# Kernel optimization log

Hardware: AMD Instinct MI355X
Metric: run time of the kernel (lower is better)

Reference implementation:

```python
import jax, jax.numpy as jnp
import numpy as np

N = 64
EPS = 1e-8


def setup_inputs() -> dict:
    key = jax.random.key(0)
    k1, k2, k3 = jax.random.split(key, 3)
    x = jax.random.normal(k1, (524288, N), dtype=jnp.float32)
    L = jax.random.uniform(k2, (2 * N, 2 * N), dtype=jnp.float32)
    R = jax.random.uniform(k3, (N, N), dtype=jnp.float32)
    return {"x": x, "L": L, "R": R}


def reference(x, L, R):
    n = N
    xr = x.reshape(n, -1)                      # (n, T)
    M = L @ L.T + EPS * jnp.eye(2 * n, dtype=L.dtype)
    M11 = M[:n, :n]
    M21 = M[:n, n:]   # note: original code names M[:n, n:] as M21
    M22 = M[n:, n:]
    A = 2.0 * (M11 + M22 + R - R.T)            # (n, n)
    A = jnp.linalg.inv(A) @ M21                # Koopman operator (n, n)
    return (A @ xr).reshape(-1, n)
```

## Files before the change

kernel.cpp:

```cpp
#include <hip/hip_runtime.h>

#define SN 524288

typedef float f32x4 __attribute__((ext_vector_type(4)));

__global__ __launch_bounds__(256) void k_buildC(const float* __restrict__ L,
                                                const float* __restrict__ R,
                                                float* __restrict__ Ct) {
  __shared__ float4 Ls[4096];
  const float4* L4 = (const float4*)L;
  #pragma unroll
  for (int it = 0; it < 16; ++it) {
    int idx = threadIdx.x + it * 256;
    int row = idx >> 5, t4 = idx & 31;
    Ls[(row << 5) + (t4 ^ (row & 7))] = L4[idx];
  }
  __syncthreads();
  int g = blockIdx.x * 256 + threadIdx.x;
  int c = g >> 6;
  int i = g & 63;
  if (c < 64) {
    float d1 = 0.f, d2 = 0.f;
    #pragma unroll
    for (int t4 = 0; t4 < 32; ++t4) {
      float4 a1 = Ls[(i << 5) + (t4 ^ (i & 7))];
      float4 b1 = Ls[(c << 5) + (t4 ^ (c & 7))];
      float4 a2 = Ls[((64 + i) << 5) + (t4 ^ (i & 7))];
      float4 b2 = Ls[((64 + c) << 5) + (t4 ^ (c & 7))];
      d1 += a1.x * b1.x + a1.y * b1.y + a1.z * b1.z + a1.w * b1.w;
      d2 += a2.x * b2.x + a2.y * b2.y + a2.z * b2.z + a2.w * b2.w;
    }
    float val = 2.0f * (d1 + d2 + R[i * 64 + c] - R[c * 64 + i]);
    if (i == c) val += 4e-8f;
    Ct[c * 64 + i] = val;
  } else {
    int jj = c - 64;
    float d = 0.f;
    #pragma unroll
    for (int t4 = 0; t4 < 32; ++t4) {
      float4 a = Ls[(i << 5) + (t4 ^ (i & 7))];
      float4 b = Ls[((64 + jj) << 5) + (t4 ^ (jj & 7))];
      d += a.x * b.x + a.y * b.y + a.z * b.z + a.w * b.w;
    }
    Ct[c * 64 + i] = d;
  }
}

__global__ __launch_bounds__(256) void k_solve(const float* __restrict__ Ct,
                                               float* __restrict__ AtW) {
  __shared__ float colbuf[2][64];
  __shared__ __align__(16) float rowbuf[2][128];
  const int r = threadIdx.x & 63;
  const int cgrp = threadIdx.x >> 6;
  float creg[32];
  #pragma unroll
  for (int cc = 0; cc < 32; ++cc)
    creg[cc] = Ct[(cgrp * 32 + cc) * 64 + r];
  #pragma unroll
  for (int p = 0; p < 64; ++p) {
    const int pb = p & 1, pc = p >> 5, pi = p & 31;
    if (cgrp == pc) colbuf[pb][r] = creg[pi];
    if (r == p) {
      #pragma unroll
      for (int cc = 0; cc < 32; ++cc) rowbuf[pb][cgrp * 32 + cc] = creg[cc];
    }
    __syncthreads();
    const float f = colbuf[pb][r];
    const float inv = 1.0f / colbuf[pb][p];
    if (r == p) {
      #pragma unroll
      for (int cc = 0; cc < 32; ++cc) creg[cc] *= inv;
    } else {
      const float gg = f * inv;
      #pragma unroll
      for (int c4 = 0; c4 < 8; ++c4) {
        const float4 pv = *(const float4*)&rowbuf[pb][cgrp * 32 + c4 * 4];
        creg[c4 * 4 + 0] -= gg * pv.x;
        creg[c4 * 4 + 1] -= gg * pv.y;
        creg[c4 * 4 + 2] -= gg * pv.z;
        creg[c4 * 4 + 3] -= gg * pv.w;
      }
    }
  }
  if (cgrp >= 2) {
    #pragma unroll
    for (int cc = 0; cc < 32; ++cc) {
      int k = (cgrp - 2) * 32 + cc;
      AtW[((r >> 5) * 64 + k) * 32 + (r & 31)] = creg[cc];
    }
  }
}

__global__ __launch_bounds__(256) void k_apply(const float* __restrict__ x,
                                               const float* __restrict__ AtW,
                                               float* __restrict__ out) {
  const int lane = threadIdx.x & 63;
  const int wv = threadIdx.x >> 6;
  const int jw = wv & 1;
  const int h = __builtin_amdgcn_readfirstlane(wv >> 1);
  const int c = blockIdx.x * 128 + jw * 64 + lane;
  const float* __restrict__ Ab = AtW + h * 64 * 32;

  float acc[32];
  #pragma unroll
  for (int i = 0; i < 32; ++i) acc[i] = 0.f;

  const float* xc = x + c;
  float xb[4];
  #pragma unroll
  for (int d = 0; d < 4; ++d) xb[d] = xc[d * SN];

  #pragma unroll 4
  for (int k = 0; k < 64; ++k) {
    const float xv = xb[k & 3];
    const int kp = (k + 4 < 64) ? (k + 4) : 63;
    xb[k & 3] = xc[kp * SN];
    const float* __restrict__ ak = Ab + k * 32;
    #pragma unroll
    for (int i = 0; i < 32; ++i)
      acc[i] = fmaf(ak[i], xv, acc[i]);
  }

  float* oc = out + (h * 32) * SN + c;
  #pragma unroll
  for (int i = 0; i < 32; ++i)
    oc[i * SN] = acc[i];
}

extern "C" void kernel_launch(void* const* d_in, const int* in_sizes, int n_in,
                              void* d_out, int out_size, void* d_ws, size_t ws_size,
                              hipStream_t stream) {
  const float* x = (const float*)d_in[0];
  const float* L = (const float*)d_in[1];
  const float* R = (const float*)d_in[2];
  float* out = (float*)d_out;
  float* Ct  = (float*)d_ws;
  float* AtW = Ct + 128 * 64;
  k_buildC<<<32, 256, 0, stream>>>(L, R, Ct);
  k_solve<<<1, 256, 0, stream>>>(Ct, AtW);
  k_apply<<<4096, 256, 0, stream>>>(x, AtW, out);
}
```

Before: 101.0 us.

## Register-block apply kernel over 4 columns with 16 output rows per wave

```diff
diff --git a/kernel.cpp b/kernel.cpp
--- a/kernel.cpp
+++ b/kernel.cpp
@@ -86,7 +86,7 @@
     #pragma unroll
     for (int cc = 0; cc < 32; ++cc) {
       int k = (cgrp - 2) * 32 + cc;
-      AtW[((r >> 5) * 64 + k) * 32 + (r & 31)] = creg[cc];
+      AtW[((r >> 4) * 64 + k) * 16 + (r & 15)] = creg[cc];
     }
   }
 }
@@ -95,36 +95,43 @@
                                                const float* __restrict__ AtW,
                                                float* __restrict__ out) {
   const int lane = threadIdx.x & 63;
-  const int wv = threadIdx.x >> 6;
-  const int jw = wv & 1;
-  const int h = __builtin_amdgcn_readfirstlane(wv >> 1);
-  const int c = blockIdx.x * 128 + jw * 64 + lane;
-  const float* __restrict__ Ab = AtW + h * 64 * 32;
+  const int h = __builtin_amdgcn_readfirstlane(threadIdx.x >> 6);
+  const int c4 = blockIdx.x * 64 + lane;
+  const float* __restrict__ Ab = AtW + h * 64 * 16;
 
-  float acc[32];
+  float acc[16][4];
   #pragma unroll
-  for (int i = 0; i < 32; ++i) acc[i] = 0.f;
+  for (int il = 0; il < 16; ++il)
+    #pragma unroll
+    for (int j = 0; j < 4; ++j) acc[il][j] = 0.f;
 
-  const float* xc = x + c;
-  float xb[4];
+  const f32x4* x4 = (const f32x4*)x;
+  f32x4 xb[4];
   #pragma unroll
-  for (int d = 0; d < 4; ++d) xb[d] = xc[d * SN];
+  for (int d = 0; d < 4; ++d) xb[d] = x4[d * (SN / 4) + c4];
 
   #pragma unroll 4
   for (int k = 0; k < 64; ++k) {
-    const float xv = xb[k & 3];
+    const f32x4 xv = xb[k & 3];
     const int kp = (k + 4 < 64) ? (k + 4) : 63;
-    xb[k & 3] = xc[kp * SN];
-    const float* __restrict__ ak = Ab + k * 32;
+    xb[k & 3] = x4[kp * (SN / 4) + c4];
+    const float* __restrict__ ak = Ab + k * 16;
     #pragma unroll
-    for (int i = 0; i < 32; ++i)
-      acc[i] = fmaf(ak[i], xv, acc[i]);
+    for (int il = 0; il < 16; ++il) {
+      const float av = ak[il];
+      acc[il][0] = fmaf(av, xv[0], acc[il][0]);
+      acc[il][1] = fmaf(av, xv[1], acc[il][1]);
+      acc[il][2] = fmaf(av, xv[2], acc[il][2]);
+      acc[il][3] = fmaf(av, xv[3], acc[il][3]);
+    }
   }
 
-  float* oc = out + (h * 32) * SN + c;
+  f32x4* out4 = (f32x4*)out;
   #pragma unroll
-  for (int i = 0; i < 32; ++i)
-    oc[i * SN] = acc[i];
+  for (int il = 0; il < 16; ++il) {
+    f32x4 v = {acc[il][0], acc[il][1], acc[il][2], acc[il][3]};
+    out4[(h * 16 + il) * (SN / 4) + c4] = v;
+  }
 }
 
 extern "C" void kernel_launch(void* const* d_in, const int* in_sizes, int n_in,
@@ -138,5 +145,5 @@
   float* AtW = Ct + 128 * 64;
   k_buildC<<<32, 256, 0, stream>>>(L, R, Ct);
   k_solve<<<1, 256, 0, stream>>>(Ct, AtW);
-  k_apply<<<4096, 256, 0, stream>>>(x, AtW, out);
+  k_apply<<<2048, 256, 0, stream>>>(x, AtW, out);
 }
```

New measurement: 103.6 us. +2.6%, slower.
